# Kernel tuning notes

Hardware: AMD Instinct MI355X
Metric: run time of the kernel (lower is better)

The kernel has to match this reference:

```python
import jax, jax.numpy as jnp
import numpy as np

N, E, H, C, F_IN, G = 20000, 320000, 8, 32, 41, 64
NEG_SLOPE = 0.2
BN_EPS = 1e-5


def setup_inputs() -> dict:
    key = jax.random.key(0)
    ks = jax.random.split(key, 32)
    s = 0.05
    d = {
        'x': jax.random.normal(ks[0], (N, F_IN), jnp.float32),
        'edge_index': jax.random.randint(ks[1], (2, E), 0, N, jnp.int32),
        'batch': jnp.sort(jax.random.randint(ks[2], (N,), 0, G, jnp.int32)),
        'graph_size': jax.random.uniform(ks[3], (G, 2), jnp.float32) * 10.0,
        'W1': jax.random.normal(ks[4], (F_IN, H * C), jnp.float32) * s,
        'a_src1': jax.random.normal(ks[5], (H, C), jnp.float32) * s,
        'a_dst1': jax.random.normal(ks[6], (H, C), jnp.float32) * s,
        'b1': jnp.zeros((H * C,), jnp.float32),
        'g1': jnp.ones((H * C,), jnp.float32),
        'be1': jnp.zeros((H * C,), jnp.float32),
        'W2': jax.random.normal(ks[7], (H * C, H * C), jnp.float32) * s,
        'a_src2': jax.random.normal(ks[8], (H, C), jnp.float32) * s,
        'a_dst2': jax.random.normal(ks[9], (H, C), jnp.float32) * s,
        'b2': jnp.zeros((H * C,), jnp.float32),
        'g2': jnp.ones((H * C,), jnp.float32),
        'be2': jnp.zeros((H * C,), jnp.float32),
        'fc1_w': jax.random.normal(ks[10], (2 * H * C + 2, 64), jnp.float32) * s,
        'fc1_b': jnp.zeros((64,), jnp.float32),
        'gf1': jnp.ones((64,), jnp.float32),
        'bf1': jnp.zeros((64,), jnp.float32),
        'fc2_w': jax.random.normal(ks[11], (64, 32), jnp.float32) * s,
        'fc2_b': jnp.zeros((32,), jnp.float32),
        'gf2': jnp.ones((32,), jnp.float32),
        'bf2': jnp.zeros((32,), jnp.float32),
        'fc3_w': jax.random.normal(ks[12], (32, 2), jnp.float32) * s,
        'fc3_b': jnp.zeros((2,), jnp.float32),
    }
    return d


def _bn_eval(x, gamma, beta):
    # eval-mode BatchNorm with running_mean=0, running_var=1
    inv = 1.0 / jnp.sqrt(1.0 + BN_EPS)
    return x * (gamma * inv) + beta


def _gat_layer(x, W, a_src, a_dst, bias, src, dst):
    h = (x @ W).reshape(N, H, C)                       # [N,H,C]
    s_src = jnp.einsum('nhc,hc->nh', h, a_src)         # [N,H]
    s_dst = jnp.einsum('nhc,hc->nh', h, a_dst)
    scores = jax.nn.leaky_relu(s_src[src] + s_dst[dst], NEG_SLOPE)  # [E+N,H]
    m = jax.ops.segment_max(scores, dst, num_segments=N)
    e = jnp.exp(scores - m[dst])
    denom = jax.ops.segment_sum(e, dst, num_segments=N)
    alpha = e / denom[dst]                             # [E+N,H]
    out = jax.ops.segment_sum(alpha[:, :, None] * h[src], dst, num_segments=N)
    return out.reshape(N, H * C) + bias


def reference(x, edge_index, batch, graph_size, W1, a_src1, a_dst1, b1, g1, be1,
              W2, a_src2, a_dst2, b2, g2, be2, fc1_w, fc1_b, gf1, bf1,
              fc2_w, fc2_b, gf2, bf2, fc3_w, fc3_b):
    # add self loops (PyG GATConv add_self_loops=True)
    loops = jnp.arange(N, dtype=edge_index.dtype)
    src = jnp.concatenate([edge_index[0], loops])
    dst = jnp.concatenate([edge_index[1], loops])

    h = _gat_layer(x, W1, a_src1, a_dst1, b1, src, dst)
    h = jax.nn.elu(_bn_eval(h, g1, be1))
    h = _gat_layer(h, W2, a_src2, a_dst2, b2, src, dst)
    h = jax.nn.elu(_bn_eval(h, g2, be2))

    # global mean + max pooling per graph
    counts = jax.ops.segment_sum(jnp.ones((N, 1), h.dtype), batch, num_segments=G)
    x_mean = jax.ops.segment_sum(h, batch, num_segments=G) / jnp.maximum(counts, 1.0)
    x_max = jax.ops.segment_max(h, batch, num_segments=G)
    p = jnp.concatenate([x_mean, x_max, graph_size], axis=1)  # [G, 514]

    z = jax.nn.relu(_bn_eval(p @ fc1_w + fc1_b, gf1, bf1))
    z = jax.nn.relu(_bn_eval(z @ fc2_w + fc2_b, gf2, bf2))
    logits = z @ fc3_w + fc3_b
    return logits
```

## Files before the change

### kernel.cpp

```cpp
#include <hip/hip_runtime.h>
#include <hip/hip_bf16.h>

#define N_NODES 20000
#define E_EDGES 320000
#define NH 8
#define NC 32
#define HC 256
#define FIN 41
#define NG 64
#define PCHUNK 16
#define NPAD 20032

typedef _Float16 f16x4 __attribute__((ext_vector_type(4)));
typedef _Float16 f16x8 __attribute__((ext_vector_type(8)));
typedef float f32x4v __attribute__((ext_vector_type(4)));


__global__ __launch_bounds__(256) void hist(const int* __restrict__ ei, int* cnt) {
    int e = blockIdx.x * 256 + threadIdx.x;
    if (e < E_EDGES) atomicAdd(&cnt[ei[E_EDGES + e]], 1);
}

__global__ __launch_bounds__(512) void scanA(const int* __restrict__ cnt, int* partial) {
    __shared__ int red[512];
    int n = blockIdx.x * 512 + threadIdx.x;
    int v = (n < N_NODES) ? cnt[n] + 1 : 0;
    red[threadIdx.x] = v; __syncthreads();
    for (int off = 256; off > 0; off >>= 1) {
        if (threadIdx.x < off) red[threadIdx.x] += red[threadIdx.x + off];
        __syncthreads();
    }
    if (threadIdx.x == 0) partial[blockIdx.x] = red[0];
}

__global__ __launch_bounds__(64) void scanB(int* partial) {
    int t = threadIdx.x;
    int v = (t < 40) ? partial[t] : 0;
    int orig = v;
    for (int off = 1; off < 64; off <<= 1) {
        int y = __shfl_up(v, off);
        if (t >= off) v += y;
    }
    if (t < 40) partial[t] = v - orig;
}

__global__ __launch_bounds__(512) void scanC(const int* __restrict__ cnt, const int* __restrict__ partial,
                                             int* row_ptr, int* cursor, int* colidx) {
    __shared__ int buf[512];
    int t = threadIdx.x;
    int n = blockIdx.x * 512 + t;
    int v = (n < N_NODES) ? cnt[n] + 1 : 0;
    int x = v;
    buf[t] = x; __syncthreads();
    for (int off = 1; off < 512; off <<= 1) {
        int y = (t >= off) ? buf[t - off] : 0;
        __syncthreads();
        x += y; buf[t] = x; __syncthreads();
    }
    int excl = partial[blockIdx.x] + x - v;
    if (n < N_NODES) {
        row_ptr[n] = excl;
        cursor[n] = excl + 1;
        colidx[excl] = n;
    }
    if (n == 0) row_ptr[N_NODES] = E_EDGES + N_NODES;
}

__global__ __launch_bounds__(256) void fill_csr(const int* __restrict__ ei, int* cursor, int* colidx) {
    int e = blockIdx.x * 256 + threadIdx.x;
    if (e >= E_EDGES) return;
    int d = ei[E_EDGES + e];
    int s = ei[e];
    int pos = atomicAdd(&cursor[d], 1);
    colidx[pos] = s;
}


__global__ __launch_bounds__(256) void prep(const float* __restrict__ W, _Float16* __restrict__ Wt,
                                            const float* __restrict__ fc1w, float* __restrict__ fc1wT,
                                            const int* __restrict__ batch, int* gstart, int* gend,
                                            const float* __restrict__ W1, _Float16* __restrict__ W1t,
                                            const float* __restrict__ x, _Float16* __restrict__ xpad) {
    __shared__ float tile[64][65];
    int b = blockIdx.x;
    int t = threadIdx.x;
    if (b < 16) {
        int tr = (b >> 2) * 64;
        int tc = (b & 3) * 64;
        int rr = t >> 6, cc = t & 63;
#pragma unroll
        for (int j = 0; j < 16; ++j) {
            int row = j * 4 + rr;
            tile[row][cc] = W[(size_t)(tr + row) * 256 + tc + cc];
        }
        __syncthreads();
#pragma unroll
        for (int j = 0; j < 16; ++j) {
            int row = j * 4 + rr;
            Wt[(size_t)(tc + row) * 256 + tr + cc] = (_Float16)tile[cc][row];
        }
    } else if (b < 145) {
        int id = (b - 16) * 256 + t;
        if (id < 64 * 514) {
            int u = id / 514, kk = id - u * 514;
            fc1wT[u * 520 + kk] = fc1w[kk * 64 + u];
        }
    } else if (b < 224) {
        int n = (b - 145) * 256 + t;
        if (n < N_NODES) {
            int bb = batch[n];
            if (n == 0) gstart[bb] = 0;
            else {
                int pb = batch[n - 1];
                if (pb != bb) { gstart[bb] = n; gend[pb] = n; }
            }
            if (n == N_NODES - 1) gend[bb] = N_NODES;
        }
    } else if (b < 288) {
        int id = (b - 224) * 256 + t;
        int n = id >> 6, k = id & 63;
        W1t[id] = (k < FIN) ? (_Float16)W1[k * 256 + n] : (_Float16)0.f;
    } else {
        int row = (b - 288) * 32 + (t >> 3);
        int c8 = (t & 7) * 8;
        f16x8 v;
#pragma unroll
        for (int j = 0; j < 8; ++j) {
            int c = c8 + j;
            float f = (row < N_NODES && c < FIN) ? x[(size_t)row * FIN + c] : 0.f;
            v[j] = (_Float16)f;
        }
        if (row < NPAD) *(f16x8*)(xpad + (size_t)row * 64 + c8) = v;
    }
}


__global__ __launch_bounds__(256) void gemm256h(const _Float16* __restrict__ Xh,
                                                const _Float16* __restrict__ Wt,
                                                const float* __restrict__ a_src,
                                                const float* __restrict__ a_dst,
                                                _Float16* __restrict__ Hh,
                                                float* __restrict__ ssrc,
                                                float* __restrict__ sdst) {
    __shared__ _Float16 bs[32 * 272];
    __shared__ _Float16 hs[64 * 40];
    int row0 = (blockIdx.x >> 3) * 64;
    int wcol = blockIdx.x & 7;
    int c0 = wcol * 32;
    int tid = threadIdx.x;
    int lane = tid & 63;
    int v = tid >> 6;
    int r16 = lane & 15;
    int kseg = lane >> 4;

#pragma unroll
    for (int i = 0; i < 4; ++i) {
        int chunk = i * 256 + tid;
        int c = chunk >> 5;
        int k = (chunk & 31) * 8;
        f16x8 xv = *(const f16x8*)(Wt + (size_t)(c0 + c) * 256 + k);
        *(f16x8*)(&bs[c * 272 + k]) = xv;
    }

    int arow = row0 + v * 16 + r16;
    const _Float16* XA = Xh + (size_t)arow * 256 + kseg * 8;
    f16x8 af[8];
#pragma unroll
    for (int s = 0; s < 8; ++s) af[s] = *(const f16x8*)(XA + s * 32);

    __syncthreads();

    f16x8 bf[2][8];
#pragma unroll
    for (int tn = 0; tn < 2; ++tn)
#pragma unroll
        for (int s = 0; s < 8; ++s)
            bf[tn][s] = *(const f16x8*)(&bs[(tn * 16 + r16) * 272 + kseg * 8 + s * 32]);

    f32x4v acc[2];
    acc[0] = (f32x4v){0.f, 0.f, 0.f, 0.f};
    acc[1] = (f32x4v){0.f, 0.f, 0.f, 0.f};
#pragma unroll
    for (int s = 0; s < 8; ++s) {
        acc[0] = __builtin_amdgcn_mfma_f32_16x16x32_f16(af[s], bf[0][s], acc[0], 0, 0, 0);
        acc[1] = __builtin_amdgcn_mfma_f32_16x16x32_f16(af[s], bf[1][s], acc[1], 0, 0, 0);
    }

    float as0 = a_src[c0 + r16], as1 = a_src[c0 + 16 + r16];
    float ad0 = a_dst[c0 + r16], ad1 = a_dst[c0 + 16 + r16];
#pragma unroll
    for (int r = 0; r < 4; ++r) {
        float p = acc[0][r] * as0 + acc[1][r] * as1;
        float q = acc[0][r] * ad0 + acc[1][r] * ad1;
        p += __shfl_xor(p, 1); q += __shfl_xor(q, 1);
        p += __shfl_xor(p, 2); q += __shfl_xor(q, 2);
        p += __shfl_xor(p, 4); q += __shfl_xor(q, 4);
        p += __shfl_xor(p, 8); q += __shfl_xor(q, 8);
        int row = row0 + v * 16 + kseg * 4 + r;
        if (r16 == 0 && row < N_NODES) {
            ssrc[row * NH + wcol] = p;
            sdst[row * NH + wcol] = q;
        }
    }

#pragma unroll
    for (int tn = 0; tn < 2; ++tn)
#pragma unroll
        for (int r = 0; r < 4; ++r)
            hs[(v * 16 + kseg * 4 + r) * 40 + tn * 16 + r16] = (_Float16)acc[tn][r];
    __syncthreads();
    {
        int row = tid >> 2;
        int c8 = (tid & 3) * 8;
        if (row0 + row < N_NODES) {
            f16x8 xv = *(const f16x8*)&hs[row * 40 + c8];
            *(f16x8*)(Hh + (size_t)(row0 + row) * 256 + c0 + c8) = xv;
        }
    }
}


__global__ __launch_bounds__(256) void gemm41h(const _Float16* __restrict__ Xh,
                                               const _Float16* __restrict__ W1t,
                                               const float* __restrict__ a_src,
                                               const float* __restrict__ a_dst,
                                               _Float16* __restrict__ Hh,
                                               float* __restrict__ ssrc,
                                               float* __restrict__ sdst) {
    __shared__ _Float16 bs[32 * 72];
    __shared__ _Float16 hs[64 * 40];
    int row0 = (blockIdx.x >> 3) * 64;
    int wcol = blockIdx.x & 7;
    int c0 = wcol * 32;
    int tid = threadIdx.x;
    int lane = tid & 63;
    int v = tid >> 6;
    int r16 = lane & 15;
    int kseg = lane >> 4;

    {
        int c = tid >> 3;
        int k = (tid & 7) * 8;
        f16x8 xv = *(const f16x8*)(W1t + (size_t)(c0 + c) * 64 + k);
        *(f16x8*)(&bs[c * 72 + k]) = xv;
    }

    int arow = row0 + v * 16 + r16;
    const _Float16* XA = Xh + (size_t)arow * 64 + kseg * 8;
    f16x8 af[2];
    af[0] = *(const f16x8*)(XA);
    af[1] = *(const f16x8*)(XA + 32);

    __syncthreads();

    f16x8 bf[2][2];
#pragma unroll
    for (int tn = 0; tn < 2; ++tn)
#pragma unroll
        for (int s = 0; s < 2; ++s)
            bf[tn][s] = *(const f16x8*)(&bs[(tn * 16 + r16) * 72 + kseg * 8 + s * 32]);

    f32x4v acc[2];
    acc[0] = (f32x4v){0.f, 0.f, 0.f, 0.f};
    acc[1] = (f32x4v){0.f, 0.f, 0.f, 0.f};
#pragma unroll
    for (int s = 0; s < 2; ++s) {
        acc[0] = __builtin_amdgcn_mfma_f32_16x16x32_f16(af[s], bf[0][s], acc[0], 0, 0, 0);
        acc[1] = __builtin_amdgcn_mfma_f32_16x16x32_f16(af[s], bf[1][s], acc[1], 0, 0, 0);
    }

    float as0 = a_src[c0 + r16], as1 = a_src[c0 + 16 + r16];
    float ad0 = a_dst[c0 + r16], ad1 = a_dst[c0 + 16 + r16];
#pragma unroll
    for (int r = 0; r < 4; ++r) {
        float p = acc[0][r] * as0 + acc[1][r] * as1;
        float q = acc[0][r] * ad0 + acc[1][r] * ad1;
        p += __shfl_xor(p, 1); q += __shfl_xor(q, 1);
        p += __shfl_xor(p, 2); q += __shfl_xor(q, 2);
        p += __shfl_xor(p, 4); q += __shfl_xor(q, 4);
        p += __shfl_xor(p, 8); q += __shfl_xor(q, 8);
        int row = row0 + v * 16 + kseg * 4 + r;
        if (r16 == 0 && row < N_NODES) {
            ssrc[row * NH + wcol] = p;
            sdst[row * NH + wcol] = q;
        }
    }

#pragma unroll
    for (int tn = 0; tn < 2; ++tn)
#pragma unroll
        for (int r = 0; r < 4; ++r)
            hs[(v * 16 + kseg * 4 + r) * 40 + tn * 16 + r16] = (_Float16)acc[tn][r];
    __syncthreads();
    {
        int row = tid >> 2;
        int c8 = (tid & 3) * 8;
        if (row0 + row < N_NODES) {
            f16x8 xv = *(const f16x8*)&hs[row * 40 + c8];
            *(f16x8*)(Hh + (size_t)(row0 + row) * 256 + c0 + c8) = xv;
        }
    }
}


__global__ __launch_bounds__(256) void gat_agg(const int* __restrict__ row_ptr,
                                               const int* __restrict__ colidx,
                                               const float* __restrict__ ssrc,
                                               const float* __restrict__ sdst,
                                               const _Float16* __restrict__ h,
                                               const float* __restrict__ bias,
                                               const float* __restrict__ gamma,
                                               const float* __restrict__ beta,
                                               _Float16* __restrict__ outh) {
    int wave = (blockIdx.x * blockDim.x + threadIdx.x) >> 6;
    int lane = threadIdx.x & 63;
    if (wave >= N_NODES) return;
    int n = wave;
    int beg = row_ptr[n], end = row_ptr[n + 1];
    int deg = end - beg;

    int hd = lane >> 3;
    float sd = sdst[n * NH + hd];
    int c = lane * 4;
    float acc0 = 0.f, acc1 = 0.f, acc2 = 0.f, acc3 = 0.f, denom = 0.f;

    int i = 0;
    for (; i + 8 <= deg; i += 8) {
        int sidx[8];
#pragma unroll
        for (int j = 0; j < 8; ++j) sidx[j] = colidx[beg + i + j];
        float wv[8];
#pragma unroll
        for (int j = 0; j < 8; ++j) {
            float v = ssrc[sidx[j] * NH + hd] + sd;
            v = (v >= 0.f) ? v : 0.2f * v;
            wv[j] = __expf(v);
        }
        f16x4 hv[8];
#pragma unroll
        for (int j = 0; j < 8; ++j) hv[j] = *reinterpret_cast<const f16x4*>(h + (size_t)sidx[j] * HC + c);
#pragma unroll
        for (int j = 0; j < 8; ++j) {
            denom += wv[j];
            acc0 += wv[j] * (float)hv[j][0];
            acc1 += wv[j] * (float)hv[j][1];
            acc2 += wv[j] * (float)hv[j][2];
            acc3 += wv[j] * (float)hv[j][3];
        }
    }
    for (; i < deg; ++i) {
        int s = colidx[beg + i];
        float v = ssrc[s * NH + hd] + sd;
        v = (v >= 0.f) ? v : 0.2f * v;
        float wgt = __expf(v);
        denom += wgt;
        const f16x4 hv = *reinterpret_cast<const f16x4*>(h + (size_t)s * HC + c);
        acc0 += wgt * (float)hv[0]; acc1 += wgt * (float)hv[1];
        acc2 += wgt * (float)hv[2]; acc3 += wgt * (float)hv[3];
    }
    float inv = 1.0f / denom;
    const float bninv = 0.99999500003749981f;
    float vals[4] = {acc0, acc1, acc2, acc3};
    f16x4 o;
#pragma unroll
    for (int j = 0; j < 4; ++j) {
        float v = vals[j] * inv + bias[c + j];
        v = v * (gamma[c + j] * bninv) + beta[c + j];
        v = (v > 0.f) ? v : (__expf(v) - 1.0f);
        o[j] = (_Float16)v;
    }
    *(f16x4*)(outh + (size_t)n * HC + c) = o;
}


__global__ __launch_bounds__(256) void pool_partial(const _Float16* __restrict__ h,
                                                    const int* __restrict__ gstart,
                                                    const int* __restrict__ gend,
                                                    float* __restrict__ psum,
                                                    float* __restrict__ pmax) {
    int g = blockIdx.x >> 4;
    int c = blockIdx.x & (PCHUNK - 1);
    int t = threadIdx.x;
    int s = gstart[g], e = gend[g];
    int len = e - s;
    int n0 = s + (int)(((long long)len * c) / PCHUNK);
    int n1 = s + (int)(((long long)len * (c + 1)) / PCHUNK);
    float sum = 0.f, mx = -3.0e38f;
    for (int n = n0; n < n1; ++n) {
        float v = (float)h[(size_t)n * HC + t];
        sum += v;
        mx = fmaxf(mx, v);
    }
    psum[(size_t)(g * PCHUNK + c) * HC + t] = sum;
    pmax[(size_t)(g * PCHUNK + c) * HC + t] = mx;
}


__global__ __launch_bounds__(256) void mlp(const float* __restrict__ psum,
                                           const float* __restrict__ pmax,
                                           const int* __restrict__ gstart,
                                           const int* __restrict__ gend,
                                           const float* __restrict__ gsz,
                                           const float* __restrict__ fc1wT, const float* __restrict__ fc1b,
                                           const float* __restrict__ gf1, const float* __restrict__ bf1,
                                           const float* __restrict__ fc2w, const float* __restrict__ fc2b,
                                           const float* __restrict__ gf2, const float* __restrict__ bf2,
                                           const float* __restrict__ fc3w, const float* __restrict__ fc3b,
                                           float* __restrict__ out) {
    __shared__ __align__(16) float pr[514];
    __shared__ float z1[64];
    __shared__ float zz2[8][32];
    __shared__ float z2[32];
    int g = blockIdx.x;
    int t = threadIdx.x;
    const float bninv = 0.99999500003749981f;

    {
        float s = 0.f, m = -3.0e38f;
#pragma unroll
        for (int c = 0; c < PCHUNK; ++c) {
            s += psum[(size_t)(g * PCHUNK + c) * HC + t];
            m = fmaxf(m, pmax[(size_t)(g * PCHUNK + c) * HC + t]);
        }
        float cnt = (float)(gend[g] - gstart[g]);
        pr[t] = s / fmaxf(cnt, 1.f);
        pr[256 + t] = m;
        if (t < 2) pr[512 + t] = gsz[g * 2 + t];
    }
    __syncthreads();

    {
        int wv = t >> 6, lane = t & 63;
        float4 pa = *reinterpret_cast<const float4*>(&pr[lane * 8]);
        float4 pb = *reinterpret_cast<const float4*>(&pr[lane * 8 + 4]);
#pragma unroll 4
        for (int i = 0; i < 16; ++i) {
            int u = wv * 16 + i;
            const float* wrow = fc1wT + u * 520;
            float4 wa = *reinterpret_cast<const float4*>(wrow + lane * 8);
            float4 wb = *reinterpret_cast<const float4*>(wrow + lane * 8 + 4);
            float a = pa.x * wa.x + pa.y * wa.y + pa.z * wa.z + pa.w * wa.w
                    + pb.x * wb.x + pb.y * wb.y + pb.z * wb.z + pb.w * wb.w;
            if (lane == 0) a += pr[512] * wrow[512] + pr[513] * wrow[513];
            a += __shfl_xor(a, 1); a += __shfl_xor(a, 2); a += __shfl_xor(a, 4);
            a += __shfl_xor(a, 8); a += __shfl_xor(a, 16); a += __shfl_xor(a, 32);
            if (lane == 0) {
                a += fc1b[u];
                a = a * (gf1[u] * bninv) + bf1[u];
                z1[u] = fmaxf(a, 0.f);
            }
        }
    }
    __syncthreads();

    {
        int u = t & 31, sp = t >> 5;
        float b = 0.f;
#pragma unroll
        for (int k = sp * 8; k < sp * 8 + 8; ++k) b += z1[k] * fc2w[k * 32 + u];
        zz2[sp][u] = b;
    }
    __syncthreads();
    if (t < 32) {
        float b = 0.f;
#pragma unroll
        for (int sp = 0; sp < 8; ++sp) b += zz2[sp][t];
        b += fc2b[t];
        b = b * (gf2[t] * bninv) + bf2[t];
        z2[t] = fmaxf(b, 0.f);
    }
    __syncthreads();

    if (t < 2) {
        float c = 0.f;
#pragma unroll
        for (int k = 0; k < 32; ++k) c += z2[k] * fc3w[k * 2 + t];
        out[g * 2 + t] = c + fc3b[t];
    }
}


extern "C" void kernel_launch(void* const* d_in, const int* in_sizes, int n_in,
                              void* d_out, int out_size, void* d_ws, size_t ws_size,
                              hipStream_t stream) {
    const float* x    = (const float*)d_in[0];
    const int*   ei   = (const int*)d_in[1];
    const int*   batch= (const int*)d_in[2];
    const float* gsz  = (const float*)d_in[3];
    const float* W1   = (const float*)d_in[4];
    const float* as1  = (const float*)d_in[5];
    const float* ad1  = (const float*)d_in[6];
    const float* b1   = (const float*)d_in[7];
    const float* g1   = (const float*)d_in[8];
    const float* be1  = (const float*)d_in[9];
    const float* W2   = (const float*)d_in[10];
    const float* as2  = (const float*)d_in[11];
    const float* ad2  = (const float*)d_in[12];
    const float* b2   = (const float*)d_in[13];
    const float* g2   = (const float*)d_in[14];
    const float* be2  = (const float*)d_in[15];
    const float* fc1w = (const float*)d_in[16];
    const float* fc1b = (const float*)d_in[17];
    const float* gf1  = (const float*)d_in[18];
    const float* bf1  = (const float*)d_in[19];
    const float* fc2w = (const float*)d_in[20];
    const float* fc2b = (const float*)d_in[21];
    const float* gf2  = (const float*)d_in[22];
    const float* bf2  = (const float*)d_in[23];
    const float* fc3w = (const float*)d_in[24];
    const float* fc3b = (const float*)d_in[25];
    float* out = (float*)d_out;

    char* w = (char*)d_ws;
    _Float16* h_half   = (_Float16*)w; w += (size_t)N_NODES * HC * 2;
    _Float16* act_half = (_Float16*)w; w += (size_t)N_NODES * HC * 2;
    _Float16* act2_half= (_Float16*)w; w += (size_t)N_NODES * HC * 2;
    _Float16* Wt       = (_Float16*)w; w += (size_t)HC * HC * 2;
    _Float16* W1t      = (_Float16*)w; w += (size_t)HC * 64 * 2;
    _Float16* xpad     = (_Float16*)w; w += (size_t)NPAD * 64 * 2;
    float* fc1wT       = (float*)w;    w += (size_t)64 * 520 * 4;
    float* ssrc        = (float*)w;    w += (size_t)N_NODES * NH * 4;
    float* sdst        = (float*)w;    w += (size_t)N_NODES * NH * 4;
    int* row_ptr  = (int*)w;   w += (size_t)(N_NODES + 1) * 4;
    int* cursor   = (int*)w;   w += (size_t)N_NODES * 4;
    int* cnt      = (int*)w;   w += (size_t)N_NODES * 4;
    int* gstart   = (int*)w;   w += 64 * 4;
    int* gend     = (int*)w;   w += 64 * 4;
    int* colidx   = (int*)w;   w += (size_t)(E_EDGES + N_NODES) * 4;
    int* partial  = (int*)w;   w += 64 * 4;

    float* psum = (float*)h_half;
    float* pmax = psum + (size_t)NG * PCHUNK * HC;

    hipMemsetAsync(cnt, 0, (size_t)(N_NODES + 128) * 4, stream);

    prep<<<914, 256, 0, stream>>>(W2, Wt, fc1w, fc1wT, batch, gstart, gend, W1, W1t, x, xpad);
    hist<<<1250, 256, 0, stream>>>(ei, cnt);
    scanA<<<40, 512, 0, stream>>>(cnt, partial);
    scanB<<<1, 64, 0, stream>>>(partial);
    scanC<<<40, 512, 0, stream>>>(cnt, partial, row_ptr, cursor, colidx);
    fill_csr<<<1250, 256, 0, stream>>>(ei, cursor, colidx);

    gemm41h<<<2504, 256, 0, stream>>>(xpad, W1t, as1, ad1, h_half, ssrc, sdst);
    gat_agg<<<5000, 256, 0, stream>>>(row_ptr, colidx, ssrc, sdst, h_half, b1, g1, be1, act_half);

    gemm256h<<<2504, 256, 0, stream>>>(act_half, Wt, as2, ad2, h_half, ssrc, sdst);
    gat_agg<<<5000, 256, 0, stream>>>(row_ptr, colidx, ssrc, sdst, h_half, b2, g2, be2, act2_half);

    pool_partial<<<NG * PCHUNK, 256, 0, stream>>>(act2_half, gstart, gend, psum, pmax);
    mlp<<<NG, 256, 0, stream>>>(psum, pmax, gstart, gend, gsz,
                                fc1wT, fc1b, gf1, bf1, fc2w, fc2b, gf2, bf2, fc3w, fc3b, out);
}
```

Measured before the change: 165.9 us.

## Widen GEMM column tiles to 128 and fold scanB into scanC

Both projection GEMM kernels now compute 128 output columns (four heads) per block instead of 32, so each 64-row A tile is loaded from global memory twice rather than eight times, and grid size drops from 2504 to 626 blocks. The LDS weight buffer is reused as the output staging buffer. Separately, the single-block partial-sum scan is merged into scanC, with each block recomputing the 40-element prefix itself, removing one kernel launch. The larger tiles raise LDS use (about 68 KB for gemm256h) and register pressure, and fewer blocks may lower occupancy.

After: 167.0 us. Within noise of the previous version (+0.7%).

```diff
diff --git a/kernel.cpp b/kernel.cpp
--- a/kernel.cpp
+++ b/kernel.cpp
@@ -33,21 +33,20 @@
     if (threadIdx.x == 0) partial[blockIdx.x] = red[0];
 }
 
-__global__ __launch_bounds__(64) void scanB(int* partial) {
-    int t = threadIdx.x;
-    int v = (t < 40) ? partial[t] : 0;
-    int orig = v;
-    for (int off = 1; off < 64; off <<= 1) {
-        int y = __shfl_up(v, off);
-        if (t >= off) v += y;
-    }
-    if (t < 40) partial[t] = v - orig;
-}
-
 __global__ __launch_bounds__(512) void scanC(const int* __restrict__ cnt, const int* __restrict__ partial,
                                              int* row_ptr, int* cursor, int* colidx) {
     __shared__ int buf[512];
+    __shared__ int pbase;
     int t = threadIdx.x;
+    if (t < 64) {
+        int v = (t < 40) ? partial[t] : 0;
+        int own = v;
+        for (int off = 1; off < 64; off <<= 1) {
+            int y = __shfl_up(v, off);
+            if (t >= off) v += y;
+        }
+        if (t == (int)blockIdx.x) pbase = v - own;
+    }
     int n = blockIdx.x * 512 + t;
     int v = (n < N_NODES) ? cnt[n] + 1 : 0;
     int x = v;
@@ -57,7 +56,7 @@
         __syncthreads();
         x += y; buf[t] = x; __syncthreads();
     }
-    int excl = partial[blockIdx.x] + x - v;
+    int excl = pbase + x - v;
     if (n < N_NODES) {
         row_ptr[n] = excl;
         cursor[n] = excl + 1;
@@ -142,11 +141,10 @@
                                                 _Float16* __restrict__ Hh,
                                                 float* __restrict__ ssrc,
                                                 float* __restrict__ sdst) {
-    __shared__ _Float16 bs[32 * 272];
-    __shared__ _Float16 hs[64 * 40];
-    int row0 = (blockIdx.x >> 3) * 64;
-    int wcol = blockIdx.x & 7;
-    int c0 = wcol * 32;
+    __shared__ _Float16 bs[128 * 272];
+    int row0 = (blockIdx.x >> 1) * 64;
+    int half = blockIdx.x & 1;
+    int c0 = half * 128;
     int tid = threadIdx.x;
     int lane = tid & 63;
     int v = tid >> 6;
@@ -154,7 +152,7 @@
     int kseg = lane >> 4;
 
 #pragma unroll
-    for (int i = 0; i < 4; ++i) {
+    for (int i = 0; i < 16; ++i) {
         int chunk = i * 256 + tid;
         int c = chunk >> 5;
         int k = (chunk & 31) * 8;
@@ -170,50 +168,56 @@
 
     __syncthreads();
 
-    f16x8 bf[2][8];
-#pragma unroll
-    for (int tn = 0; tn < 2; ++tn)
+    f32x4v acc[8];
+#pragma unroll
+    for (int tn = 0; tn < 8; ++tn) acc[tn] = (f32x4v){0.f, 0.f, 0.f, 0.f};
+
+#pragma unroll
+    for (int tn = 0; tn < 8; ++tn) {
+        f16x8 bf[8];
 #pragma unroll
         for (int s = 0; s < 8; ++s)
-            bf[tn][s] = *(const f16x8*)(&bs[(tn * 16 + r16) * 272 + kseg * 8 + s * 32]);
-
-    f32x4v acc[2];
-    acc[0] = (f32x4v){0.f, 0.f, 0.f, 0.f};
-    acc[1] = (f32x4v){0.f, 0.f, 0.f, 0.f};
-#pragma unroll
-    for (int s = 0; s < 8; ++s) {
-        acc[0] = __builtin_amdgcn_mfma_f32_16x16x32_f16(af[s], bf[0][s], acc[0], 0, 0, 0);
-        acc[1] = __builtin_amdgcn_mfma_f32_16x16x32_f16(af[s], bf[1][s], acc[1], 0, 0, 0);
-    }
-
-    float as0 = a_src[c0 + r16], as1 = a_src[c0 + 16 + r16];
-    float ad0 = a_dst[c0 + r16], ad1 = a_dst[c0 + 16 + r16];
-#pragma unroll
-    for (int r = 0; r < 4; ++r) {
-        float p = acc[0][r] * as0 + acc[1][r] * as1;
-        float q = acc[0][r] * ad0 + acc[1][r] * ad1;
-        p += __shfl_xor(p, 1); q += __shfl_xor(q, 1);
-        p += __shfl_xor(p, 2); q += __shfl_xor(q, 2);
-        p += __shfl_xor(p, 4); q += __shfl_xor(q, 4);
-        p += __shfl_xor(p, 8); q += __shfl_xor(q, 8);
-        int row = row0 + v * 16 + kseg * 4 + r;
-        if (r16 == 0 && row < N_NODES) {
-            ssrc[row * NH + wcol] = p;
-            sdst[row * NH + wcol] = q;
-        }
-    }
-
-#pragma unroll
-    for (int tn = 0; tn < 2; ++tn)
+            bf[s] = *(const f16x8*)(&bs[(tn * 16 + r16) * 272 + kseg * 8 + s * 32]);
+#pragma unroll
+        for (int s = 0; s < 8; ++s)
+            acc[tn] = __builtin_amdgcn_mfma_f32_16x16x32_f16(af[s], bf[s], acc[tn], 0, 0, 0);
+    }
+
+#pragma unroll
+    for (int hh = 0; hh < 4; ++hh) {
+        float as0 = a_src[c0 + hh * 32 + r16], as1 = a_src[c0 + hh * 32 + 16 + r16];
+        float ad0 = a_dst[c0 + hh * 32 + r16], ad1 = a_dst[c0 + hh * 32 + 16 + r16];
+#pragma unroll
+        for (int r = 0; r < 4; ++r) {
+            float p = acc[2 * hh][r] * as0 + acc[2 * hh + 1][r] * as1;
+            float q = acc[2 * hh][r] * ad0 + acc[2 * hh + 1][r] * ad1;
+            p += __shfl_xor(p, 1); q += __shfl_xor(q, 1);
+            p += __shfl_xor(p, 2); q += __shfl_xor(q, 2);
+            p += __shfl_xor(p, 4); q += __shfl_xor(q, 4);
+            p += __shfl_xor(p, 8); q += __shfl_xor(q, 8);
+            int row = row0 + v * 16 + kseg * 4 + r;
+            if (r16 == 0 && row < N_NODES) {
+                ssrc[row * NH + half * 4 + hh] = p;
+                sdst[row * NH + half * 4 + hh] = q;
+            }
+        }
+    }
+
+    __syncthreads();
+    _Float16* hs = bs;
+#pragma unroll
+    for (int tn = 0; tn < 8; ++tn)
 #pragma unroll
         for (int r = 0; r < 4; ++r)
-            hs[(v * 16 + kseg * 4 + r) * 40 + tn * 16 + r16] = (_Float16)acc[tn][r];
-    __syncthreads();
-    {
-        int row = tid >> 2;
-        int c8 = (tid & 3) * 8;
+            hs[(v * 16 + kseg * 4 + r) * 136 + tn * 16 + r16] = (_Float16)acc[tn][r];
+    __syncthreads();
+#pragma unroll
+    for (int i = 0; i < 4; ++i) {
+        int idx = i * 256 + tid;
+        int row = idx >> 4;
+        int c8 = (idx & 15) * 8;
         if (row0 + row < N_NODES) {
-            f16x8 xv = *(const f16x8*)&hs[row * 40 + c8];
+            f16x8 xv = *(const f16x8*)&hs[row * 136 + c8];
             *(f16x8*)(Hh + (size_t)(row0 + row) * 256 + c0 + c8) = xv;
         }
     }
@@ -227,20 +231,21 @@
                                                _Float16* __restrict__ Hh,
                                                float* __restrict__ ssrc,
                                                float* __restrict__ sdst) {
-    __shared__ _Float16 bs[32 * 72];
-    __shared__ _Float16 hs[64 * 40];
-    int row0 = (blockIdx.x >> 3) * 64;
-    int wcol = blockIdx.x & 7;
-    int c0 = wcol * 32;
+    __shared__ _Float16 bs[128 * 72];
+    int row0 = (blockIdx.x >> 1) * 64;
+    int half = blockIdx.x & 1;
+    int c0 = half * 128;
     int tid = threadIdx.x;
     int lane = tid & 63;
     int v = tid >> 6;
     int r16 = lane & 15;
     int kseg = lane >> 4;
 
-    {
-        int c = tid >> 3;
-        int k = (tid & 7) * 8;
+#pragma unroll
+    for (int i = 0; i < 4; ++i) {
+        int chunk = i * 256 + tid;
+        int c = chunk >> 3;
+        int k = (chunk & 7) * 8;
         f16x8 xv = *(const f16x8*)(W1t + (size_t)(c0 + c) * 64 + k);
         *(f16x8*)(&bs[c * 72 + k]) = xv;
     }
@@ -253,50 +258,53 @@
 
     __syncthreads();
 
-    f16x8 bf[2][2];
-#pragma unroll
-    for (int tn = 0; tn < 2; ++tn)
-#pragma unroll
-        for (int s = 0; s < 2; ++s)
-            bf[tn][s] = *(const f16x8*)(&bs[(tn * 16 + r16) * 72 + kseg * 8 + s * 32]);
-
-    f32x4v acc[2];
-    acc[0] = (f32x4v){0.f, 0.f, 0.f, 0.f};
-    acc[1] = (f32x4v){0.f, 0.f, 0.f, 0.f};
-#pragma unroll
-    for (int s = 0; s < 2; ++s) {
-        acc[0] = __builtin_amdgcn_mfma_f32_16x16x32_f16(af[s], bf[0][s], acc[0], 0, 0, 0);
-        acc[1] = __builtin_amdgcn_mfma_f32_16x16x32_f16(af[s], bf[1][s], acc[1], 0, 0, 0);
-    }
-
-    float as0 = a_src[c0 + r16], as1 = a_src[c0 + 16 + r16];
-    float ad0 = a_dst[c0 + r16], ad1 = a_dst[c0 + 16 + r16];
-#pragma unroll
-    for (int r = 0; r < 4; ++r) {
-        float p = acc[0][r] * as0 + acc[1][r] * as1;
-        float q = acc[0][r] * ad0 + acc[1][r] * ad1;
-        p += __shfl_xor(p, 1); q += __shfl_xor(q, 1);
-        p += __shfl_xor(p, 2); q += __shfl_xor(q, 2);
-        p += __shfl_xor(p, 4); q += __shfl_xor(q, 4);
-        p += __shfl_xor(p, 8); q += __shfl_xor(q, 8);
-        int row = row0 + v * 16 + kseg * 4 + r;
-        if (r16 == 0 && row < N_NODES) {
-            ssrc[row * NH + wcol] = p;
-            sdst[row * NH + wcol] = q;
-        }
-    }
-
-#pragma unroll
-    for (int tn = 0; tn < 2; ++tn)
+    f32x4v acc[8];
+#pragma unroll
+    for (int tn = 0; tn < 8; ++tn) acc[tn] = (f32x4v){0.f, 0.f, 0.f, 0.f};
+
+#pragma unroll
+    for (int tn = 0; tn < 8; ++tn) {
+        f16x8 bf0 = *(const f16x8*)(&bs[(tn * 16 + r16) * 72 + kseg * 8]);
+        f16x8 bf1 = *(const f16x8*)(&bs[(tn * 16 + r16) * 72 + kseg * 8 + 32]);
+        acc[tn] = __builtin_amdgcn_mfma_f32_16x16x32_f16(af[0], bf0, acc[tn], 0, 0, 0);
+        acc[tn] = __builtin_amdgcn_mfma_f32_16x16x32_f16(af[1], bf1, acc[tn], 0, 0, 0);
+    }
+
+#pragma unroll
+    for (int hh = 0; hh < 4; ++hh) {
+        float as0 = a_src[c0 + hh * 32 + r16], as1 = a_src[c0 + hh * 32 + 16 + r16];
+        float ad0 = a_dst[c0 + hh * 32 + r16], ad1 = a_dst[c0 + hh * 32 + 16 + r16];
+#pragma unroll
+        for (int r = 0; r < 4; ++r) {
+            float p = acc[2 * hh][r] * as0 + acc[2 * hh + 1][r] * as1;
+            float q = acc[2 * hh][r] * ad0 + acc[2 * hh + 1][r] * ad1;
+            p += __shfl_xor(p, 1); q += __shfl_xor(q, 1);
+            p += __shfl_xor(p, 2); q += __shfl_xor(q, 2);
+            p += __shfl_xor(p, 4); q += __shfl_xor(q, 4);
+            p += __shfl_xor(p, 8); q += __shfl_xor(q, 8);
+            int row = row0 + v * 16 + kseg * 4 + r;
+            if (r16 == 0 && row < N_NODES) {
+                ssrc[row * NH + half * 4 + hh] = p;
+                sdst[row * NH + half * 4 + hh] = q;
+            }
+        }
+    }
+
+    __syncthreads();
+    _Float16* hs = bs;
+#pragma unroll
+    for (int tn = 0; tn < 8; ++tn)
 #pragma unroll
         for (int r = 0; r < 4; ++r)
-            hs[(v * 16 + kseg * 4 + r) * 40 + tn * 16 + r16] = (_Float16)acc[tn][r];
-    __syncthreads();
-    {
-        int row = tid >> 2;
-        int c8 = (tid & 3) * 8;
+            hs[(v * 16 + kseg * 4 + r) * 136 + tn * 16 + r16] = (_Float16)acc[tn][r];
+    __syncthreads();
+#pragma unroll
+    for (int i = 0; i < 4; ++i) {
+        int idx = i * 256 + tid;
+        int row = idx >> 4;
+        int c8 = (idx & 15) * 8;
         if (row0 + row < N_NODES) {
-            f16x8 xv = *(const f16x8*)&hs[row * 40 + c8];
+            f16x8 xv = *(const f16x8*)&hs[row * 136 + c8];
             *(f16x8*)(Hh + (size_t)(row0 + row) * 256 + c0 + c8) = xv;
         }
     }
@@ -537,14 +545,13 @@
     prep<<<914, 256, 0, stream>>>(W2, Wt, fc1w, fc1wT, batch, gstart, gend, W1, W1t, x, xpad);
     hist<<<1250, 256, 0, stream>>>(ei, cnt);
     scanA<<<40, 512, 0, stream>>>(cnt, partial);
-    scanB<<<1, 64, 0, stream>>>(partial);
     scanC<<<40, 512, 0, stream>>>(cnt, partial, row_ptr, cursor, colidx);
     fill_csr<<<1250, 256, 0, stream>>>(ei, cursor, colidx);
 
-    gemm41h<<<2504, 256, 0, stream>>>(xpad, W1t, as1, ad1, h_half, ssrc, sdst);
+    gemm41h<<<626, 256, 0, stream>>>(xpad, W1t, as1, ad1, h_half, ssrc, sdst);
     gat_agg<<<5000, 256, 0, stream>>>(row_ptr, colidx, ssrc, sdst, h_half, b1, g1, be1, act_half);
 
-    gemm256h<<<2504, 256, 0, stream>>>(act_half, Wt, as2, ad2, h_half, ssrc, sdst);
+    gemm256h<<<626, 256, 0, stream>>>(act_half, Wt, as2, ad2, h_half, ssrc, sdst);
     gat_agg<<<5000, 256, 0, stream>>>(row_ptr, colidx, ssrc, sdst, h_half, b2, g2, be2, act2_half);
 
     pool_partial<<<NG * PCHUNK, 256, 0, stream>>>(act2_half, gstart, gend, psum, pmax);
```
